# Optimization experiments

Measured on AMD Instinct MI355X. Metric: run time of the kernel, lower is better.

## Reference

```python
import jax, jax.numpy as jnp
import numpy as np

N_NODES = 100000
N_EDGES = 1600000
IN_C, HID_C, OUT_C = 165, 256, 2


def setup_inputs() -> dict:
    key = jax.random.key(0)
    ks = jax.random.split(key, 7)
    x = jax.random.normal(ks[0], (N_NODES, IN_C), dtype=jnp.float32)
    edge_index = jax.random.randint(ks[1], (2, N_EDGES), 0, N_NODES, dtype=jnp.int64)
    # Glorot-ish scaled weights
    W1_l = jax.random.normal(ks[2], (IN_C, HID_C), dtype=jnp.float32) / np.sqrt(IN_C)
    W1_r = jax.random.normal(ks[3], (IN_C, HID_C), dtype=jnp.float32) / np.sqrt(IN_C)
    W2_l = jax.random.normal(ks[4], (HID_C, OUT_C), dtype=jnp.float32) / np.sqrt(HID_C)
    W2_r = jax.random.normal(ks[5], (HID_C, OUT_C), dtype=jnp.float32) / np.sqrt(HID_C)
    b1 = jnp.zeros((HID_C,), dtype=jnp.float32)
    b2 = jnp.zeros((OUT_C,), dtype=jnp.float32)
    return {"x": x, "edge_index": edge_index, "W1_l": W1_l, "b1": b1,
            "W1_r": W1_r, "W2_l": W2_l, "b2": b2, "W2_r": W2_r}


def _sage_conv(h, src, dst, n_nodes, Wl, b, Wr):
    # mean aggregation of neighbor messages (src -> dst), as in PyG SAGEConv
    agg = jax.ops.segment_sum(h[src], dst, num_segments=n_nodes)  # [N, C]
    deg = jax.ops.segment_sum(jnp.ones_like(dst, dtype=h.dtype), dst,
                              num_segments=n_nodes)               # [N]
    mean = agg / jnp.maximum(deg, 1.0)[:, None]
    # out = lin_l(aggr) + lin_r(root); bias lives on lin_l
    return mean @ Wl + b + h @ Wr


def reference(x, edge_index, W1_l, b1, W1_r, W2_l, b2, W2_r):
    src, dst = edge_index[0], edge_index[1]
    n = x.shape[0]
    h = jax.nn.relu(_sage_conv(x, src, dst, n, W1_l, b1, W1_r))
    out = _sage_conv(h, src, dst, n, W2_l, b2, W2_r)
    return out
```

## Files before the change

kernel.cpp:

```cpp
#include <hip/hip_runtime.h>

#define N_NODES 100000
#define N_EDGES 1600000
#define IN_C 165
#define HID_C 256
#define OUT_C 2

#define XPAD 168
#define LDSROW 360
#define NBLK_SCAN 98

typedef short bf16x8 __attribute__((ext_vector_type(8)));
typedef float f32x4 __attribute__((ext_vector_type(4)));

__device__ inline unsigned short f2bf(float f) {
    unsigned int u = __float_as_uint(f);
    u += 0x7fffu + ((u >> 16) & 1u);
    return (unsigned short)(u >> 16);
}
__device__ inline float bf2f(unsigned short h) {
    return __uint_as_float(((unsigned int)h) << 16);
}
__device__ inline unsigned int pack2bf(float a, float b) {
    return (unsigned int)f2bf(a) | ((unsigned int)f2bf(b) << 16);
}


__launch_bounds__(1024)
__global__ void k_scan1(const int* __restrict__ deg, int* __restrict__ incl,
                        int* __restrict__ btot) {
    const int tid = threadIdx.x;
    const int idx = blockIdx.x * 1024 + tid;
    const int lane = tid & 63, wid = tid >> 6;
    __shared__ int ws[16];
    int v = (idx < N_NODES) ? deg[idx] : 0;
    int s = v;
#pragma unroll
    for (int off = 1; off < 64; off <<= 1) {
        int t = __shfl_up(s, off);
        if (lane >= off) s += t;
    }
    if (lane == 63) ws[wid] = s;
    __syncthreads();
    if (wid == 0) {
        int p = (lane < 16) ? ws[lane] : 0;
#pragma unroll
        for (int off = 1; off < 16; off <<= 1) {
            int t = __shfl_up(p, off);
            if (lane >= off) p += t;
        }
        if (lane < 16) ws[lane] = p;
    }
    __syncthreads();
    int blockincl = s + (wid > 0 ? ws[wid - 1] : 0);
    if (idx < N_NODES) incl[idx] = blockincl;
    if (tid == 1023) btot[blockIdx.x] = blockincl;
}

__global__ void k_scan2(int* __restrict__ btot) {
    const int lane = threadIdx.x;
    int a = (2 * lane < NBLK_SCAN) ? btot[2 * lane] : 0;
    int b = (2 * lane + 1 < NBLK_SCAN) ? btot[2 * lane + 1] : 0;
    int p = a + b;
#pragma unroll
    for (int off = 1; off < 64; off <<= 1) {
        int t = __shfl_up(p, off);
        if (lane >= off) p += t;
    }
    if (2 * lane < NBLK_SCAN) btot[2 * lane] = p - b;
    if (2 * lane + 1 < NBLK_SCAN) btot[2 * lane + 1] = p;
}

__launch_bounds__(1024)
__global__ void k_scan3(const int* __restrict__ deg, int* incl_cursor,
                        const int* __restrict__ btot, int* __restrict__ rowptr) {
    const int idx = blockIdx.x * 1024 + threadIdx.x;
    if (idx == 0) rowptr[0] = 0;
    if (idx >= N_NODES) return;
    int off = (blockIdx.x > 0) ? btot[blockIdx.x - 1] : 0;
    int v = incl_cursor[idx] + off;
    rowptr[idx + 1] = v;
    incl_cursor[idx] = v - deg[idx];
}

__global__ void k_fill(const int* __restrict__ src, const int* __restrict__ dst,
                       int* __restrict__ cursor, int* __restrict__ csr) {
    int e = blockIdx.x * blockDim.x + threadIdx.x;
    if (e >= N_EDGES) return;
    int d = dst[e];
    int pos = atomicAdd(&cursor[d], 1);
    csr[pos] = src[e];
}

__global__ void k_cvt(const float* __restrict__ x, const int* __restrict__ dst,
                      uint2* __restrict__ xb2, int* __restrict__ deg) {
    int idx = blockIdx.x * blockDim.x + threadIdx.x;
    if (idx < N_EDGES) atomicAdd(&deg[dst[idx]], 1);
    if (idx >= N_NODES * 42) return;
    int n = idx / 42;
    int t = idx - n * 42;
    int c = 4 * t;
    float f0 = x[(size_t)n * IN_C + c];
    float f1 = (c + 1 < IN_C) ? x[(size_t)n * IN_C + c + 1] : 0.f;
    float f2 = (c + 2 < IN_C) ? x[(size_t)n * IN_C + c + 2] : 0.f;
    float f3 = (c + 3 < IN_C) ? x[(size_t)n * IN_C + c + 3] : 0.f;
    uint2 p;
    p.x = pack2bf(f0, f1);
    p.y = pack2bf(f2, f3);
    xb2[idx] = p;
}

__global__ void k_wt(const float* __restrict__ W1l, const float* __restrict__ W1r,
                     unsigned short* __restrict__ Wt) {
    int k = blockIdx.x;
    int c = threadIdx.x;
    float v = 0.0f;
    if (k < IN_C) v = W1l[k * HID_C + c];
    else if (k >= XPAD && k < XPAD + IN_C) v = W1r[(k - XPAD) * HID_C + c];
    Wt[(size_t)c * 352 + k] = f2bf(v);
}

__global__ void k_agg1b(const int* __restrict__ rowptr, const int* __restrict__ csr,
                        const uint2* __restrict__ xb2, uint2* __restrict__ aggb2) {
    int n = (blockIdx.x * blockDim.x + threadIdx.x) >> 6;
    if (n >= N_NODES) return;
    const int lane = threadIdx.x & 63;
    const bool act = lane < 42;
    int beg = rowptr[n], end = rowptr[n + 1];
    float a0 = 0.f, a1 = 0.f, a2 = 0.f, a3 = 0.f;
    int j = beg;
#define ACC(u) { a0 += bf2f((unsigned short)((u).x & 0xffffu)); \
                 a1 += bf2f((unsigned short)((u).x >> 16)); \
                 a2 += bf2f((unsigned short)((u).y & 0xffffu)); \
                 a3 += bf2f((unsigned short)((u).y >> 16)); }
    for (; j + 3 < end; j += 4) {
        int s0 = csr[j], s1 = csr[j + 1], s2 = csr[j + 2], s3 = csr[j + 3];
        uint2 u0 = make_uint2(0, 0), u1 = make_uint2(0, 0);
        uint2 u2 = make_uint2(0, 0), u3 = make_uint2(0, 0);
        if (act) {
            u0 = xb2[(size_t)s0 * 42 + lane];
            u1 = xb2[(size_t)s1 * 42 + lane];
            u2 = xb2[(size_t)s2 * 42 + lane];
            u3 = xb2[(size_t)s3 * 42 + lane];
        }
        ACC(u0); ACC(u1); ACC(u2); ACC(u3);
    }
    for (; j < end; ++j) {
        int s0 = csr[j];
        uint2 u0 = act ? xb2[(size_t)s0 * 42 + lane] : make_uint2(0, 0);
        ACC(u0);
    }
#undef ACC
    if (act) {
        float invd = 1.0f / fmaxf((float)(end - beg), 1.0f);
        uint2 p;
        p.x = pack2bf(a0 * invd, a1 * invd);
        p.y = pack2bf(a2 * invd, a3 * invd);
        aggb2[(size_t)n * 42 + lane] = p;
    }
}

__launch_bounds__(256)
__global__ void k_gemm1(const unsigned short* __restrict__ aggb,
                        const unsigned short* __restrict__ xb,
                        const unsigned short* __restrict__ Wt,
                        const float* __restrict__ b1,
                        const float* __restrict__ W2l, const float* __restrict__ W2r,
                        float* __restrict__ yz) {
    __shared__ __align__(16) unsigned short lds[64 * LDSROW];
    const int tid = threadIdx.x;
    const int lane = tid & 63;
    const int w = tid >> 6;
    const int node0 = blockIdx.x * 64;

#pragma unroll
    for (int it = 0; it < 12; ++it) {
        int idx = tid + it * 256;
        if (idx < 64 * 45) {
            int row = idx / 45;
            int c = idx - row * 45;
            int n = node0 + row;
            uint4 v = make_uint4(0, 0, 0, 0);
            if (n < N_NODES) {
                if (c < 21)      v = *(const uint4*)&aggb[(size_t)n * XPAD + c * 8];
                else if (c < 42) v = *(const uint4*)&xb[(size_t)n * XPAD + (c - 21) * 8];
            }
            *(uint4*)&lds[row * LDSROW + c * 8] = v;
        }
    }
    __syncthreads();

    const int arow = lane & 15;
    const int kgrp = lane >> 4;
    const int colbase = w * 64;
    f32x4 acc[4][4] = {};

    for (int ks = 0; ks < 11; ++ks) {
        const int k0 = ks * 32 + kgrp * 8;
        bf16x8 bfr[4], afr[4];
#pragma unroll
        for (int n = 0; n < 4; ++n)
            bfr[n] = *(const bf16x8*)&Wt[(size_t)(colbase + n * 16 + arow) * 352 + k0];
#pragma unroll
        for (int m = 0; m < 4; ++m)
            afr[m] = *(const bf16x8*)&lds[(m * 16 + arow) * LDSROW + k0];
#pragma unroll
        for (int m = 0; m < 4; ++m)
#pragma unroll
            for (int n = 0; n < 4; ++n)
                acc[m][n] = __builtin_amdgcn_mfma_f32_16x16x32_bf16(afr[m], bfr[n],
                                                                    acc[m][n], 0, 0, 0);
    }

    float b1c[4];
    float2 wl[4], wr[4];
#pragma unroll
    for (int n = 0; n < 4; ++n) {
        int c = colbase + n * 16 + arow;
        b1c[n] = b1[c];
        wl[n] = *(const float2*)&W2l[c * 2];
        wr[n] = *(const float2*)&W2r[c * 2];
    }
    __syncthreads();
    float* part = (float*)lds;

#pragma unroll
    for (int m = 0; m < 4; ++m)
#pragma unroll
        for (int r = 0; r < 4; ++r) {
            float y0 = 0.f, y1 = 0.f, z0 = 0.f, z1 = 0.f;
#pragma unroll
            for (int n = 0; n < 4; ++n) {
                float h = fmaxf(acc[m][n][r] + b1c[n], 0.0f);
                y0 = fmaf(h, wl[n].x, y0); y1 = fmaf(h, wl[n].y, y1);
                z0 = fmaf(h, wr[n].x, z0); z1 = fmaf(h, wr[n].y, z1);
            }
#pragma unroll
            for (int off = 1; off < 16; off <<= 1) {
                y0 += __shfl_xor(y0, off); y1 += __shfl_xor(y1, off);
                z0 += __shfl_xor(z0, off); z1 += __shfl_xor(z1, off);
            }
            if (arow == 0) {
                int row = m * 16 + kgrp * 4 + r;
                float* p = &part[(w * 64 + row) * 4];
                p[0] = y0; p[1] = y1; p[2] = z0; p[3] = z1;
            }
        }
    __syncthreads();

    {
        int row = tid >> 2;
        int ch = tid & 3;
        float s = part[row * 4 + ch] + part[(256 + row * 4) + ch] +
                  part[(512 + row * 4) + ch] + part[(768 + row * 4) + ch];
        int node = node0 + row;
        if (node < N_NODES) yz[(size_t)node * 4 + ch] = s;
    }
}

__global__ void k_layer2(const int* __restrict__ rowptr, const int* __restrict__ csr,
                         const float* __restrict__ yz, const float* __restrict__ b2,
                         float* __restrict__ out) {
    int n = (blockIdx.x * blockDim.x + threadIdx.x) >> 6;
    if (n >= N_NODES) return;
    const int lane = threadIdx.x & 63;
    int beg = rowptr[n], end = rowptr[n + 1];
    float y0 = 0.f, y1 = 0.f;
    for (int i = beg + lane; i < end; i += 64) {
        int s = csr[i];
        float2 v = *(const float2*)&yz[(size_t)s * 4];
        y0 += v.x; y1 += v.y;
    }
#pragma unroll
    for (int off = 32; off >= 1; off >>= 1) {
        y0 += __shfl_xor(y0, off);
        y1 += __shfl_xor(y1, off);
    }
    if (lane == 0) {
        float invd = 1.0f / fmaxf((float)(end - beg), 1.0f);
        float2 o;
        o.x = y0 * invd + b2[0] + yz[(size_t)n * 4 + 2];
        o.y = y1 * invd + b2[1] + yz[(size_t)n * 4 + 3];
        *(float2*)&out[n * 2] = o;
    }
}

extern "C" void kernel_launch(void* const* d_in, const int* in_sizes, int n_in,
                              void* d_out, int out_size, void* d_ws, size_t ws_size,
                              hipStream_t stream) {
    const float* x   = (const float*)d_in[0];
    const int*   ei  = (const int*)d_in[1];
    const int*   src = ei;
    const int*   dst = ei + N_EDGES;
    const float* W1l = (const float*)d_in[2];
    const float* b1  = (const float*)d_in[3];
    const float* W1r = (const float*)d_in[4];
    const float* W2l = (const float*)d_in[5];
    const float* b2  = (const float*)d_in[6];
    const float* W2r = (const float*)d_in[7];
    float* out = (float*)d_out;

    int* wsi = (int*)d_ws;
    int* csr    = wsi;
    int* rowptr = wsi + 1600000;
    unsigned short* xb   = (unsigned short*)(wsi + 1700004);
    unsigned short* aggb = xb + (size_t)N_NODES * XPAD;
    unsigned short* Wt   = aggb + (size_t)N_NODES * XPAD;
    float* yz            = (float*)(Wt + 256 * 352);
    int* deg    = (int*)yz;
    int* inccur = (int*)yz + N_NODES;
    int* btot   = (int*)yz + 2 * N_NODES;

    hipMemsetAsync(deg, 0, N_NODES * sizeof(int), stream);

    k_cvt<<<(N_NODES * 42 + 255) / 256, 256, 0, stream>>>(x, dst, (uint2*)xb, deg);
    k_wt<<<352, 256, 0, stream>>>(W1l, W1r, Wt);
    k_scan1<<<NBLK_SCAN, 1024, 0, stream>>>(deg, inccur, btot);
    k_scan2<<<1, 64, 0, stream>>>(btot);
    k_scan3<<<NBLK_SCAN, 1024, 0, stream>>>(deg, inccur, btot, rowptr);
    k_fill<<<(N_EDGES + 255) / 256, 256, 0, stream>>>(src, dst, inccur, csr);
    k_agg1b<<<(N_NODES * 64 + 255) / 256, 256, 0, stream>>>(rowptr, csr,
                                                            (const uint2*)xb,
                                                            (uint2*)aggb);
    k_gemm1<<<(N_NODES + 63) / 64, 256, 0, stream>>>(aggb, xb, Wt, b1, W2l, W2r, yz);
    k_layer2<<<(N_NODES * 64 + 255) / 256, 256, 0, stream>>>(rowptr, csr, yz, b2, out);
}
```

Baseline: 492.8 us.

## Partition CSR fill by destination range per XCD and deepen gather unroll

The CSR fill kernel now uses a fixed grid where each block, keyed by blockIdx mod 8, handles only destinations in one eighth of the node range. Each edge is read by eight blocks, and the block that owns its destination performs the atomic and the write. The apparent aim is to keep cursor atomics and csr writes local to one XCD's L2 cache, since blocks are dispatched round-robin across XCDs, at the cost of reading src/dst eight times. The layer-1 aggregation loop also gains an 8-way unrolled gather so more neighbor loads are in flight.

```diff
diff --git a/kernel.cpp b/kernel.cpp
--- a/kernel.cpp
+++ b/kernel.cpp
@@ -83,13 +83,22 @@
     incl_cursor[idx] = v - deg[idx];
 }
 
+#define FILL_GRID 2048
 __global__ void k_fill(const int* __restrict__ src, const int* __restrict__ dst,
                        int* __restrict__ cursor, int* __restrict__ csr) {
-    int e = blockIdx.x * blockDim.x + threadIdx.x;
-    if (e >= N_EDGES) return;
-    int d = dst[e];
-    int pos = atomicAdd(&cursor[d], 1);
-    csr[pos] = src[e];
+    const int role = blockIdx.x & 7;
+    const int nchunk = gridDim.x >> 3;
+    const int lo = role * (N_NODES / 8);
+    const int hi = lo + (N_NODES / 8);
+    for (int e = (blockIdx.x >> 3) * 256 + threadIdx.x; e < N_EDGES;
+         e += nchunk * 256) {
+        int d = dst[e];
+        int s = src[e];
+        if (d >= lo && d < hi) {
+            int pos = atomicAdd(&cursor[d], 1);
+            csr[pos] = s;
+        }
+    }
 }
 
 __global__ void k_cvt(const float* __restrict__ x, const int* __restrict__ dst,
@@ -133,17 +142,25 @@
                  a1 += bf2f((unsigned short)((u).x >> 16)); \
                  a2 += bf2f((unsigned short)((u).y & 0xffffu)); \
                  a3 += bf2f((unsigned short)((u).y >> 16)); }
+    for (; j + 7 < end; j += 8) {
+        uint2 u[8];
+#pragma unroll
+        for (int q = 0; q < 8; ++q) {
+            int s = csr[j + q];
+            u[q] = act ? xb2[(size_t)s * 42 + lane] : make_uint2(0, 0);
+        }
+#pragma unroll
+        for (int q = 0; q < 8; ++q) ACC(u[q]);
+    }
     for (; j + 3 < end; j += 4) {
-        int s0 = csr[j], s1 = csr[j + 1], s2 = csr[j + 2], s3 = csr[j + 3];
-        uint2 u0 = make_uint2(0, 0), u1 = make_uint2(0, 0);
-        uint2 u2 = make_uint2(0, 0), u3 = make_uint2(0, 0);
-        if (act) {
-            u0 = xb2[(size_t)s0 * 42 + lane];
-            u1 = xb2[(size_t)s1 * 42 + lane];
-            u2 = xb2[(size_t)s2 * 42 + lane];
-            u3 = xb2[(size_t)s3 * 42 + lane];
-        }
-        ACC(u0); ACC(u1); ACC(u2); ACC(u3);
+        uint2 u[4];
+#pragma unroll
+        for (int q = 0; q < 4; ++q) {
+            int s = csr[j + q];
+            u[q] = act ? xb2[(size_t)s * 42 + lane] : make_uint2(0, 0);
+        }
+#pragma unroll
+        for (int q = 0; q < 4; ++q) ACC(u[q]);
     }
     for (; j < end; ++j) {
         int s0 = csr[j];
@@ -318,7 +335,7 @@
     k_scan1<<<NBLK_SCAN, 1024, 0, stream>>>(deg, inccur, btot);
     k_scan2<<<1, 64, 0, stream>>>(btot);
     k_scan3<<<NBLK_SCAN, 1024, 0, stream>>>(deg, inccur, btot, rowptr);
-    k_fill<<<(N_EDGES + 255) / 256, 256, 0, stream>>>(src, dst, inccur, csr);
+    k_fill<<<FILL_GRID, 256, 0, stream>>>(src, dst, inccur, csr);
     k_agg1b<<<(N_NODES * 64 + 255) / 256, 256, 0, stream>>>(rowptr, csr,
                                                             (const uint2*)xb,
                                                             (uint2*)aggb);
```

Result: faster. 466.3 us (-5.4%).
